# Optimization experiments

Hardware: AMD Instinct MI355X
Metric: run time of the kernel (lower is better)

Reference implementation:

```python
import jax, jax.numpy as jnp
import numpy as np

NUM_HEADS = 8
KERNEL = 7
LOW_RANK = 4


def setup_inputs() -> dict:
    key = jax.random.key(0)
    ks = jax.random.split(key, 10)
    B, H, W, C = 4, 56, 56, 256
    nh, K, lr = NUM_HEADS, KERNEL, LOW_RANK
    s = 0.02
    return {
        "x": jax.random.normal(ks[0], (B, H, W, C), jnp.float32),
        "Wq": jax.random.normal(ks[1], (C, nh * lr), jnp.float32) * s,
        "bq": jnp.zeros((nh * lr,), jnp.float32),
        "Wk": jax.random.normal(ks[2], (C, nh * lr), jnp.float32) * s,
        "bk": jnp.zeros((nh * lr,), jnp.float32),
        "Wv": jax.random.normal(ks[3], (C, C), jnp.float32) * s,
        "bv": jnp.zeros((C,), jnp.float32),
        "rpb": jax.random.normal(ks[4], (nh, 2 * K - 1, 2 * K - 1), jnp.float32) * s,
        "Wp": jax.random.normal(ks[5], (C, C), jnp.float32) * s,
        "bp": jnp.zeros((C,), jnp.float32),
    }


def reference(x, Wq, bq, Wk, bk, Wv, bv, rpb, Wp, bp):
    B, H, W, C = x.shape
    nh, K, lr = NUM_HEADS, KERNEL, LOW_RANK
    hd = C // nh
    r = K // 2
    scale = hd ** -0.5

    # Projections. Note: the original uses a raw reshape (B,H,W,nh*lr)->(B,nh,H,W,lr),
    # which we replicate exactly (row-major reshape, no permute).
    q = (x @ Wq + bq).reshape(B, nh, H, W, lr) * scale
    k = (x @ Wk + bk).reshape(B, nh, H, W, lr)
    v = (x @ Wv + bv).reshape(B, nh, H, W, hd)

    # NATTEN window start indices (clamped so each query sees exactly K keys per axis).
    start_h = jnp.clip(jnp.arange(H) - r, 0, H - K)  # (H,)
    start_w = jnp.clip(jnp.arange(W) - r, 0, W - K)  # (W,)
    idx_h = start_h[:, None] + jnp.arange(K)[None, :]  # (H, K)
    idx_w = start_w[:, None] + jnp.arange(K)[None, :]  # (W, K)

    # Gather local K/V windows: (B, nh, H, K, W, K, d)
    k_win = k[:, :, idx_h][:, :, :, :, idx_w]
    v_win = v[:, :, idx_h][:, :, :, :, idx_w]

    # Scores: (B, nh, H, W, K, K)
    attn = jnp.einsum('bhijc,bhikjlc->bhijkl', q, k_win)

    # Relative position bias indices: (key_pos - query_pos) + (K-1)
    bi = idx_h - jnp.arange(H)[:, None] + (K - 1)  # (H, K)
    bj = idx_w - jnp.arange(W)[:, None] + (K - 1)  # (W, K)
    bias = rpb[:, bi][:, :, :, bj]                 # (nh, H, K, W, K)
    attn = attn + bias.transpose(0, 1, 3, 2, 4)[None]  # (B, nh, H, W, K, K)

    attn = jax.nn.softmax(attn.reshape(B, nh, H, W, K * K), axis=-1)
    attn = attn.reshape(B, nh, H, W, K, K)

    # Weighted aggregation of V windows: (B, nh, H, W, hd)
    out = jnp.einsum('bhijkl,bhikjld->bhijd', attn, v_win)
    out = out.transpose(0, 2, 3, 1, 4).reshape(B, H, W, C)
    return out @ Wp + bp
```

## Files before the change

### kernel.cpp

```cpp
#include <hip/hip_runtime.h>
#include <hip/hip_bf16.h>

#define BD 4
#define HD_ 56
#define WD 56
#define CD 256
#define NH 8
#define KW 7
#define LR 4
#define HDIM 32
#define MB (HD_*WD)
#define NROWS (BD*MB)
#define QK_PER_B (HD_*WD*32)
#define V_PER_B  (HD_*WD*256)

typedef short short8 __attribute__((ext_vector_type(8)));
typedef float floatx4 __attribute__((ext_vector_type(4)));

static __device__ inline ushort f2bf(float f) {
    __hip_bfloat16 h = __float2bfloat16(f);
    return *(ushort*)&h;
}
static __device__ inline float bf2f(uint h16) {
    union { uint u; float f; } c; c.u = h16 << 16; return c.f;
}
static __device__ inline float bf2f_hi(uint u) {
    union { uint v; float f; } c; c.v = u & 0xffff0000u; return c.f;
}

typedef const __attribute__((address_space(1))) void* gp1_t;
typedef __attribute__((address_space(3))) void* sp3_t;
static __device__ __forceinline__ void glds16(const void* g, void* s) {
    __builtin_amdgcn_global_load_lds((gp1_t)g, (sp3_t)s, 16, 0, 0);
}

__global__ __launch_bounds__(256) void prep_all(
    const float* __restrict__ x,
    const float* __restrict__ Wq, const float* __restrict__ Wk,
    const float* __restrict__ Wv, const float* __restrict__ bq,
    const float* __restrict__ bk, const float* __restrict__ bv,
    const float* __restrict__ Wp,
    ushort* __restrict__ xb, ushort* __restrict__ WpkT,
    ushort* __restrict__ WpT, float* __restrict__ pb)
{
    int idx = blockIdx.x * 256 + threadIdx.x;
    if (idx < 401408) {
        float4 f0 = *(const float4*)&x[idx * 8];
        float4 f1 = *(const float4*)&x[idx * 8 + 4];
        union { ushort h[8]; uint4 u; } p;
        p.h[0] = f2bf(f0.x); p.h[1] = f2bf(f0.y); p.h[2] = f2bf(f0.z); p.h[3] = f2bf(f0.w);
        p.h[4] = f2bf(f1.x); p.h[5] = f2bf(f1.y); p.h[6] = f2bf(f1.z); p.h[7] = f2bf(f1.w);
        *(uint4*)&xb[idx * 8] = p.u;
    } else if (idx < 401408 + 81920) {
        int j = idx - 401408;
        int n = j >> 8, k = j & 255;
        float v;
        if (n < 32)       v = Wq[k * 32 + n];
        else if (n < 64)  v = Wk[k * 32 + (n - 32)];
        else              v = Wv[k * 256 + (n - 64)];
        WpkT[j] = f2bf(v);
    } else if (idx < 401408 + 81920 + 65536) {
        int j = idx - (401408 + 81920);
        int n = j >> 8, k = j & 255;
        WpT[j] = f2bf(Wp[k * 256 + n]);
    } else if (idx < 401408 + 81920 + 65536 + 320) {
        int n = idx - (401408 + 81920 + 65536);
        pb[n] = (n < 32) ? bq[n] : (n < 64) ? bk[n - 32] : bv[n - 64];
    }
}

static __device__ __forceinline__ void gemm_core_128x64(
    const ushort* __restrict__ Ag, const ushort* __restrict__ Bg,
    ushort* As, ushort* Bs, int m0, int n0, int t, floatx4 (&acc)[4][2])
{
    const int lane = t & 63, w = t >> 6;
    const int lx = lane & 7, ly = lane >> 3;
    const int koff = (lx ^ ly) << 3;
    const int col = lane & 15, quad = lane >> 4;
    const int swz = (col & 7) << 4;
    const int wm = w >> 1, wn = w & 1;
    char* Ac = (char*)As;
    char* Bc = (char*)Bs;

    for (int k0 = 0; k0 < 256; k0 += 64) {
        __syncthreads();
#pragma unroll
        for (int l = 0; l < 4; ++l) {
            int c = (w << 2) + l;
            int row = (c << 3) + ly;
            glds16(&Ag[(m0 + row) * 256 + k0 + koff], &As[c << 9]);
        }
#pragma unroll
        for (int l = 0; l < 2; ++l) {
            int c = (w << 1) + l;
            int row = (c << 3) + ly;
            glds16(&Bg[(n0 + row) * 256 + k0 + koff], &Bs[c << 9]);
        }
        __syncthreads();
#pragma unroll
        for (int kk = 0; kk < 2; ++kk) {
            const int kx = ((kk << 6) + (quad << 4)) ^ swz;
            short8 b0 = *(short8*)(Bc + ((wn << 5) + col) * 128 + kx);
            short8 b1 = *(short8*)(Bc + ((wn << 5) + 16 + col) * 128 + kx);
#pragma unroll
            for (int mt = 0; mt < 4; ++mt) {
                short8 a = *(short8*)(Ac + ((wm << 6) + (mt << 4) + col) * 128 + kx);
                acc[mt][0] = __builtin_amdgcn_mfma_f32_16x16x32_bf16(a, b0, acc[mt][0], 0, 0, 0);
                acc[mt][1] = __builtin_amdgcn_mfma_f32_16x16x32_bf16(a, b1, acc[mt][1], 0, 0, 0);
            }
        }
    }
}

__global__ __launch_bounds__(256) void mfma_qkv(
    const ushort* __restrict__ xb, const ushort* __restrict__ Bt,
    const float* __restrict__ pb, ushort* __restrict__ Qb,
    ushort* __restrict__ Kb, ushort* __restrict__ Vb)
{
    __shared__ ushort As[128 * 64];
    __shared__ ushort Bs[64 * 64];
    const int t = threadIdx.x;
    const int m0 = blockIdx.y * 128, n0 = blockIdx.x * 64;

    floatx4 acc[4][2] = {};
    gemm_core_128x64(xb, Bt, As, Bs, m0, n0, t, acc);

    const int lane = t & 63, w = t >> 6;
    const int col = lane & 15, quad = lane >> 4;
    const int wm = w >> 1, wn = w & 1;
#pragma unroll
    for (int mt = 0; mt < 4; ++mt) {
#pragma unroll
        for (int nt = 0; nt < 2; ++nt) {
            int gn = n0 + (wn << 5) + (nt << 4) + col;
            float bias = pb[gn];
#pragma unroll
            for (int rg = 0; rg < 4; ++rg) {
                int m = m0 + (wm << 6) + (mt << 4) + (quad << 2) + rg;
                ushort h = f2bf(acc[mt][nt][rg] + bias);
                if (gn < 32)        Qb[m * 32 + gn] = h;
                else if (gn < 64)   Kb[m * 32 + (gn - 32)] = h;
                else                Vb[m * 256 + (gn - 64)] = h;
            }
        }
    }
}

__global__ __launch_bounds__(256) void mfma_out(
    const ushort* __restrict__ Ag, const ushort* __restrict__ Bt,
    const float* __restrict__ bp, float* __restrict__ out)
{
    __shared__ ushort As[128 * 64];
    __shared__ ushort Bs[64 * 64];
    const int t = threadIdx.x;
    const int m0 = blockIdx.y * 128, n0 = blockIdx.x * 64;

    floatx4 acc[4][2] = {};
    gemm_core_128x64(Ag, Bt, As, Bs, m0, n0, t, acc);

    const int lane = t & 63, w = t >> 6;
    const int col = lane & 15, quad = lane >> 4;
    const int wm = w >> 1, wn = w & 1;
#pragma unroll
    for (int mt = 0; mt < 4; ++mt) {
#pragma unroll
        for (int nt = 0; nt < 2; ++nt) {
            int gn = n0 + (wn << 5) + (nt << 4) + col;
            float bias = bp[gn];
#pragma unroll
            for (int rg = 0; rg < 4; ++rg) {
                int m = m0 + (wm << 6) + (mt << 4) + (quad << 2) + rg;
                out[m * 256 + gn] = acc[mt][nt][rg] + bias;
            }
        }
    }
}

__global__ __launch_bounds__(256, 5) void natten_attn_t(
    const ushort* __restrict__ Qb, const ushort* __restrict__ Kb,
    const ushort* __restrict__ Vb, const float* __restrict__ rpb,
    ushort* __restrict__ Ab)
{
    __shared__ float4 Ksf[196];
    __shared__ float4 Vsf[8 * 197];
    __shared__ float  Rs[169];

    const int tj = blockIdx.x, ti = blockIdx.y;
    const int n = blockIdx.z & 7, b = blockIdx.z >> 3;
    const int t = threadIdx.x;
    const int i0 = ti * 8, j0 = tj * 8;
    const int rs = min(max(i0 - 3, 0), HD_ - 14);
    const int cs = min(max(j0 - 3, 0), WD - 14);

    const ushort* kb = Kb + b * QK_PER_B + n * (HD_ * WD * LR);
    const ushort* vb = Vb + b * V_PER_B + n * (HD_ * WD * HDIM);

    if (t < 196) {
        int r = t / 14, c = t % 14;
        union { uint2 u; uint w[2]; } kr;
        kr.u = *(const uint2*)&kb[(rs + r) * (WD * LR) + (cs + c) * LR];
        Ksf[t] = make_float4(bf2f(kr.w[0] & 0xffff), bf2f_hi(kr.w[0]),
                             bf2f(kr.w[1] & 0xffff), bf2f_hi(kr.w[1]));
    }
    if (t < 169) Rs[t] = rpb[n * 169 + t];
    for (int idx = t; idx < 784; idx += 256) {
        int oct = idx & 3, pos = idx >> 2;
        int r = pos / 14, c = pos % 14;
        union { uint4 u; uint w[4]; } vr;
        vr.u = *(const uint4*)&vb[(rs + r) * (WD * HDIM) + (cs + c) * HDIM + oct * 8];
        Vsf[(2 * oct) * 197 + pos] =
            make_float4(bf2f(vr.w[0] & 0xffff), bf2f_hi(vr.w[0]),
                        bf2f(vr.w[1] & 0xffff), bf2f_hi(vr.w[1]));
        Vsf[(2 * oct + 1) * 197 + pos] =
            make_float4(bf2f(vr.w[2] & 0xffff), bf2f_hi(vr.w[2]),
                        bf2f(vr.w[3] & 0xffff), bf2f_hi(vr.w[3]));
    }
    __syncthreads();

    const int q  = t >> 2, p = t & 3;
    const int qi = q >> 3, qj = q & 7;
    const int i = i0 + qi, j = j0 + qj;
    const int sh = min(max(i - 3, 0), HD_ - KW);
    const int sw = min(max(j - 3, 0), WD - KW);
    const int oh = sh - rs, ow = sw - cs;

    union { uint2 u; uint w[2]; } qr;
    qr.u = *(const uint2*)&Qb[b * QK_PER_B + n * (HD_ * WD * LR) + i * (WD * LR) + j * LR];
    const float scale = 0.17677669529663687f;
    float qx = bf2f(qr.w[0] & 0xffff) * scale, qy = bf2f_hi(qr.w[0]) * scale;
    float qz = bf2f(qr.w[1] & 0xffff) * scale, qw = bf2f_hi(qr.w[1]) * scale;

    const int rb0 = (sh - i + 6) * 13 + (sw - j + 6);

    float sum = 0.f;
    float a[8] = {0.f, 0.f, 0.f, 0.f, 0.f, 0.f, 0.f, 0.f};
    const float4* v0 = &Vsf[(2 * p) * 197];
    const float4* v1 = &Vsf[(2 * p + 1) * 197];
    for (int kh = 0; kh < KW; ++kh) {
        int kpos  = (oh + kh) * 14 + ow;
        int rbase = rb0 + kh * 13;
#pragma unroll
        for (int kw = 0; kw < KW; ++kw) {
            float4 kf = Ksf[kpos + kw];
            float d = Rs[rbase + kw];
            d = fmaf(qx, kf.x, d);
            d = fmaf(qy, kf.y, d);
            d = fmaf(qz, kf.z, d);
            d = fmaf(qw, kf.w, d);
            float e = __expf(d);
            sum += e;
            float4 x0 = v0[kpos + kw];
            float4 x1 = v1[kpos + kw];
            a[0] = fmaf(e, x0.x, a[0]); a[1] = fmaf(e, x0.y, a[1]);
            a[2] = fmaf(e, x0.z, a[2]); a[3] = fmaf(e, x0.w, a[3]);
            a[4] = fmaf(e, x1.x, a[4]); a[5] = fmaf(e, x1.y, a[5]);
            a[6] = fmaf(e, x1.z, a[6]); a[7] = fmaf(e, x1.w, a[7]);
        }
    }
    float inv = 1.0f / sum;

    union { ushort h[8]; uint4 u; } pk;
#pragma unroll
    for (int c = 0; c < 8; ++c) pk.h[c] = f2bf(a[c] * inv);
    *(uint4*)&Ab[(((b * HD_ + i) * WD + j)) * CD + n * HDIM + p * 8] = pk.u;
}

extern "C" void kernel_launch(void* const* d_in, const int* in_sizes, int n_in,
                              void* d_out, int out_size, void* d_ws, size_t ws_size,
                              hipStream_t stream) {
    const float* x   = (const float*)d_in[0];
    const float* Wq  = (const float*)d_in[1];
    const float* bq  = (const float*)d_in[2];
    const float* Wk  = (const float*)d_in[3];
    const float* bk  = (const float*)d_in[4];
    const float* Wv  = (const float*)d_in[5];
    const float* bv  = (const float*)d_in[6];
    const float* rpb = (const float*)d_in[7];
    const float* Wp  = (const float*)d_in[8];
    const float* bp  = (const float*)d_in[9];
    float* out = (float*)d_out;

    ushort* WpkT = (ushort*)d_ws;
    ushort* WpT  = WpkT + 81920;
    ushort* Ab   = WpT + 65536;
    ushort* Qb   = Ab + 3211264;
    ushort* Kb   = Qb + BD * QK_PER_B;
    ushort* Vb   = Kb + BD * QK_PER_B;
    ushort* xb   = Vb + BD * V_PER_B;
    float*  pb   = (float*)(xb + 3211264);

    prep_all<<<(549184 + 255) / 256, 256, 0, stream>>>(
        x, Wq, Wk, Wv, bq, bk, bv, Wp, xb, WpkT, WpT, pb);

    mfma_qkv<<<dim3(5, NROWS / 128), 256, 0, stream>>>(xb, WpkT, pb, Qb, Kb, Vb);

    natten_attn_t<<<dim3(7, 7, 32), 256, 0, stream>>>(Qb, Kb, Vb, rpb, Ab);

    mfma_out<<<dim3(4, NROWS / 128), 256, 0, stream>>>(Ab, WpT, bp, out);
}
```

Measured before the change: 117.3 us.

## Compute neighborhood attention PV aggregation with bf16 MFMA over dense tile probabilities

The attention kernel now writes each query's unnormalized exp scores into a zero-filled 64x196 (padded to 232) bf16 probability matrix in LDS covering the block's 14x14 key tile. The P·V product then runs on MFMA 16x16x32 bf16 instead of per-thread scalar FMAs. Score computation is split across the 4 threads per query by kernel row, with a shuffle reduction for the softmax sum. Global loads of V/K/rpb/Q are issued before zero-filling LDS to overlap latency. The cost is extra LDS (lower occupancy bound of 3), dense work over mostly-zero entries, bf16 rounding of probabilities, and extra syncs.

```diff
diff --git a/kernel.cpp b/kernel.cpp
--- a/kernel.cpp
+++ b/kernel.cpp
@@ -176,14 +176,16 @@
     }
 }
 
-__global__ __launch_bounds__(256, 5) void natten_attn_t(
+__global__ __launch_bounds__(256, 3) void natten_attn_m(
     const ushort* __restrict__ Qb, const ushort* __restrict__ Kb,
     const ushort* __restrict__ Vb, const float* __restrict__ rpb,
     ushort* __restrict__ Ab)
 {
+    __shared__ ushort Pl[64 * 232];
+    __shared__ ushort Vt[32 * 232];
     __shared__ float4 Ksf[196];
-    __shared__ float4 Vsf[8 * 197];
     __shared__ float  Rs[169];
+    __shared__ float  invS[64];
 
     const int tj = blockIdx.x, ti = blockIdx.y;
     const int n = blockIdx.z & 7, b = blockIdx.z >> 3;
@@ -195,74 +197,118 @@
     const ushort* kb = Kb + b * QK_PER_B + n * (HD_ * WD * LR);
     const ushort* vb = Vb + b * V_PER_B + n * (HD_ * WD * HDIM);
 
+    uint4 vreg[4];
+#pragma unroll
+    for (int it = 0; it < 4; ++it) {
+        int idx = t + it * 256;
+        if (idx < 784) {
+            int pos = idx >> 2, oct = idx & 3;
+            int r = pos / 14, c = pos % 14;
+            vreg[it] = *(const uint4*)&vb[(rs + r) * (WD * HDIM) + (cs + c) * HDIM + oct * 8];
+        }
+    }
+    uint2 kreg = make_uint2(0u, 0u);
     if (t < 196) {
         int r = t / 14, c = t % 14;
-        union { uint2 u; uint w[2]; } kr;
-        kr.u = *(const uint2*)&kb[(rs + r) * (WD * LR) + (cs + c) * LR];
-        Ksf[t] = make_float4(bf2f(kr.w[0] & 0xffff), bf2f_hi(kr.w[0]),
-                             bf2f(kr.w[1] & 0xffff), bf2f_hi(kr.w[1]));
-    }
-    if (t < 169) Rs[t] = rpb[n * 169 + t];
-    for (int idx = t; idx < 784; idx += 256) {
-        int oct = idx & 3, pos = idx >> 2;
-        int r = pos / 14, c = pos % 14;
-        union { uint4 u; uint w[4]; } vr;
-        vr.u = *(const uint4*)&vb[(rs + r) * (WD * HDIM) + (cs + c) * HDIM + oct * 8];
-        Vsf[(2 * oct) * 197 + pos] =
-            make_float4(bf2f(vr.w[0] & 0xffff), bf2f_hi(vr.w[0]),
-                        bf2f(vr.w[1] & 0xffff), bf2f_hi(vr.w[1]));
-        Vsf[(2 * oct + 1) * 197 + pos] =
-            make_float4(bf2f(vr.w[2] & 0xffff), bf2f_hi(vr.w[2]),
-                        bf2f(vr.w[3] & 0xffff), bf2f_hi(vr.w[3]));
-    }
-    __syncthreads();
+        kreg = *(const uint2*)&kb[(rs + r) * (WD * LR) + (cs + c) * LR];
+    }
+    float rreg = (t < 169) ? rpb[n * 169 + t] : 0.f;
 
     const int q  = t >> 2, p = t & 3;
     const int qi = q >> 3, qj = q & 7;
     const int i = i0 + qi, j = j0 + qj;
+    uint2 qr2 = *(const uint2*)&Qb[b * QK_PER_B + n * (HD_ * WD * LR) + i * (WD * LR) + j * LR];
+
+#pragma unroll
+    for (int it = 0; it < 8; ++it) {
+        int idx = t + (it << 8);
+        if (idx < 1856) *(uint4*)&Pl[idx << 3] = make_uint4(0, 0, 0, 0);
+    }
+#pragma unroll
+    for (int it = 0; it < 4; ++it) {
+        int idx = t + (it << 8);
+        if (idx < 928) *(uint4*)&Vt[idx << 3] = make_uint4(0, 0, 0, 0);
+    }
+    __syncthreads();
+
+    if (t < 196) {
+        Ksf[t] = make_float4(bf2f(kreg.x & 0xffff), bf2f_hi(kreg.x),
+                             bf2f(kreg.y & 0xffff), bf2f_hi(kreg.y));
+    }
+    if (t < 169) Rs[t] = rreg;
+#pragma unroll
+    for (int it = 0; it < 4; ++it) {
+        int idx = t + it * 256;
+        if (idx < 784) {
+            int pos = idx >> 2, oct = idx & 3;
+            ushort* cp = &Vt[(oct * 8) * 232 + pos];
+            union { uint4 u; ushort h[8]; } vv; vv.u = vreg[it];
+#pragma unroll
+            for (int e = 0; e < 8; ++e) cp[e * 232] = vv.h[e];
+        }
+    }
+    __syncthreads();
+
     const int sh = min(max(i - 3, 0), HD_ - KW);
     const int sw = min(max(j - 3, 0), WD - KW);
     const int oh = sh - rs, ow = sw - cs;
-
-    union { uint2 u; uint w[2]; } qr;
-    qr.u = *(const uint2*)&Qb[b * QK_PER_B + n * (HD_ * WD * LR) + i * (WD * LR) + j * LR];
     const float scale = 0.17677669529663687f;
-    float qx = bf2f(qr.w[0] & 0xffff) * scale, qy = bf2f_hi(qr.w[0]) * scale;
-    float qz = bf2f(qr.w[1] & 0xffff) * scale, qw = bf2f_hi(qr.w[1]) * scale;
-
+    float qx = bf2f(qr2.x & 0xffff) * scale, qy = bf2f_hi(qr2.x) * scale;
+    float qz = bf2f(qr2.y & 0xffff) * scale, qw = bf2f_hi(qr2.y) * scale;
     const int rb0 = (sh - i + 6) * 13 + (sw - j + 6);
 
     float sum = 0.f;
-    float a[8] = {0.f, 0.f, 0.f, 0.f, 0.f, 0.f, 0.f, 0.f};
-    const float4* v0 = &Vsf[(2 * p) * 197];
-    const float4* v1 = &Vsf[(2 * p + 1) * 197];
-    for (int kh = 0; kh < KW; ++kh) {
-        int kpos  = (oh + kh) * 14 + ow;
-        int rbase = rb0 + kh * 13;
-#pragma unroll
-        for (int kw = 0; kw < KW; ++kw) {
-            float4 kf = Ksf[kpos + kw];
-            float d = Rs[rbase + kw];
-            d = fmaf(qx, kf.x, d);
-            d = fmaf(qy, kf.y, d);
-            d = fmaf(qz, kf.z, d);
-            d = fmaf(qw, kf.w, d);
-            float e = __expf(d);
-            sum += e;
-            float4 x0 = v0[kpos + kw];
-            float4 x1 = v1[kpos + kw];
-            a[0] = fmaf(e, x0.x, a[0]); a[1] = fmaf(e, x0.y, a[1]);
-            a[2] = fmaf(e, x0.z, a[2]); a[3] = fmaf(e, x0.w, a[3]);
-            a[4] = fmaf(e, x1.x, a[4]); a[5] = fmaf(e, x1.y, a[5]);
-            a[6] = fmaf(e, x1.z, a[6]); a[7] = fmaf(e, x1.w, a[7]);
-        }
-    }
-    float inv = 1.0f / sum;
-
-    union { ushort h[8]; uint4 u; } pk;
-#pragma unroll
-    for (int c = 0; c < 8; ++c) pk.h[c] = f2bf(a[c] * inv);
-    *(uint4*)&Ab[(((b * HD_ + i) * WD + j)) * CD + n * HDIM + p * 8] = pk.u;
+#pragma unroll
+    for (int half = 0; half < 2; ++half) {
+        int kh = p + (half << 2);
+        if (kh < 7) {
+            int kpos  = (oh + kh) * 14 + ow;
+            int rbase = rb0 + kh * 13;
+            ushort* prow = &Pl[q * 232 + kpos];
+#pragma unroll
+            for (int kw = 0; kw < 7; ++kw) {
+                float4 kf = Ksf[kpos + kw];
+                float d = Rs[rbase + kw];
+                d = fmaf(qx, kf.x, d);
+                d = fmaf(qy, kf.y, d);
+                d = fmaf(qz, kf.z, d);
+                d = fmaf(qw, kf.w, d);
+                float e = __expf(d);
+                sum += e;
+                prow[kw] = f2bf(e);
+            }
+        }
+    }
+    sum += __shfl_xor(sum, 1);
+    sum += __shfl_xor(sum, 2);
+    if (p == 0) invS[q] = 1.0f / sum;
+    __syncthreads();
+
+    const int lane = t & 63, w = t >> 6;
+    const int col = lane & 15, quad = lane >> 4;
+    floatx4 acc0 = {0.f, 0.f, 0.f, 0.f}, acc1 = {0.f, 0.f, 0.f, 0.f};
+    const ushort* arow = &Pl[(w * 16 + col) * 232];
+    const ushort* b0p  = &Vt[col * 232];
+    const ushort* b1p  = &Vt[(col + 16) * 232];
+#pragma unroll
+    for (int s = 0; s < 7; ++s) {
+        int ko = s * 32 + quad * 8;
+        short8 a  = *(const short8*)(arow + ko);
+        short8 f0 = *(const short8*)(b0p + ko);
+        short8 f1 = *(const short8*)(b1p + ko);
+        acc0 = __builtin_amdgcn_mfma_f32_16x16x32_bf16(a, f0, acc0, 0, 0, 0);
+        acc1 = __builtin_amdgcn_mfma_f32_16x16x32_bf16(a, f1, acc1, 0, 0, 0);
+    }
+
+#pragma unroll
+    for (int rg = 0; rg < 4; ++rg) {
+        int qq = w * 16 + quad * 4 + rg;
+        float iv = invS[qq];
+        int ii = i0 + (qq >> 3), jj = j0 + (qq & 7);
+        ushort* dst = &Ab[(((b * HD_ + ii) * WD + jj)) * CD + n * HDIM + col];
+        dst[0]  = f2bf(acc0[rg] * iv);
+        dst[16] = f2bf(acc1[rg] * iv);
+    }
 }
 
 extern "C" void kernel_launch(void* const* d_in, const int* in_sizes, int n_in,
@@ -294,7 +340,7 @@
 
     mfma_qkv<<<dim3(5, NROWS / 128), 256, 0, stream>>>(xb, WpkT, pb, Qb, Kb, Vb);
 
-    natten_attn_t<<<dim3(7, 7, 32), 256, 0, stream>>>(Qb, Kb, Vb, rpb, Ab);
+    natten_attn_m<<<dim3(7, 7, 32), 256, 0, stream>>>(Qb, Kb, Vb, rpb, Ab);
 
     mfma_out<<<dim3(4, NROWS / 128), 256, 0, stream>>>(Ab, WpT, bp, out);
 }
```

After: 114.6 us. -2.4%, faster.
